# Kernel optimization log

Hardware: AMD Instinct MI355X
Metric: run time of the kernel (lower is better)

## Reference

```python
import jax, jax.numpy as jnp
import numpy as np
from jax.scipy.special import logsumexp

SCALE = 10.0
EPS = 1e-05
MARGIN_INTRA = 40.0
MARGIN_INTER = 6.0
K_INTRA = 4   # sorted1[4:]
K_INTER = 6   # sorted2[6:]


def setup_inputs() -> dict:
    key = jax.random.key(0)
    k1, k2 = jax.random.split(key)
    n, d, n_cams = 4096, 256, 8
    feature = jax.random.normal(k1, (n, d), dtype=jnp.float32)
    camid = jax.random.randint(k2, (n,), 0, n_cams, dtype=jnp.int64)
    return {"feature": feature, "camid": camid}


def reference(feature, camid):
    n = feature.shape[0]
    # pairwise Euclidean distances: ||fi||^2 + ||fj||^2 - 2 fi.fj + eps, clamped, sqrt
    sq = jnp.sum(feature * feature, axis=1)                      # [n]
    dist = sq[:, None] + sq[None, :] + EPS - 2.0 * (feature @ feature.T)
    dist = jnp.sqrt(jnp.clip(dist, 1e-12))                       # [n, n]

    same_cam = camid[:, None] == camid[None, :]                  # [n, n] bool
    inf = jnp.array(jnp.inf, dtype=dist.dtype)

    # masked sorts: +inf padding sorts to the end and contributes exp(-inf)=0
    sorted_intra = jnp.sort(jnp.where(same_cam, dist, inf), axis=1)   # [n, n]
    sorted_inter = jnp.sort(jnp.where(same_cam, inf, dist), axis=1)   # [n, n]

    # x = log(sum(exp(-scale * sorted[:1]))) == -scale * sorted[0]
    x_intra = -SCALE * sorted_intra[:, 0]
    y_intra = logsumexp(-SCALE * sorted_intra[:, K_INTRA:], axis=1)
    x_inter = -SCALE * sorted_inter[:, 0]
    y_inter = logsumexp(-SCALE * sorted_inter[:, K_INTER:], axis=1)

    loss_intra = jnp.sum(jnp.maximum(-x_intra + y_intra + MARGIN_INTRA, 0.0))
    loss_inter = jnp.sum(jnp.maximum(-x_inter + y_inter + MARGIN_INTER, 0.0))
    return (loss_intra + 0.5 * loss_inter) / n
```

## Files before the change

kernel.cpp:

```cpp
#include <hip/hip_runtime.h>
#include <hip/hip_bf16.h>
#include <math.h>

#define N 4096
#define D 256
#define SCALEF 10.0f
#define EPSF 1e-5f
#define MARGIN_INTRA 40.0f
#define MARGIN_INTER 6.0f
#define K_INTRA 4
#define K_INTER 6

typedef unsigned short ushort_t;
typedef __attribute__((ext_vector_type(8))) short short8;
typedef __attribute__((ext_vector_type(4))) float floatx4;

__device__ __forceinline__ ushort_t f2bf(float x) {
    __hip_bfloat16 h = __float2bfloat16(x);
    return *reinterpret_cast<ushort_t*>(&h);
}
__device__ __forceinline__ float bf2f(ushort_t u) {
    __hip_bfloat16 h = *reinterpret_cast<__hip_bfloat16*>(&u);
    return __bfloat162float(h);
}

__global__ __launch_bounds__(64) void sqnorm_kernel(const float* __restrict__ F,
                                                    float* __restrict__ sq) {
    int row = blockIdx.x;
    int lane = threadIdx.x;
    float4 v = ((const float4*)(F + (size_t)row * D))[lane];
    float s = v.x * v.x + v.y * v.y + v.z * v.z + v.w * v.w;
#pragma unroll
    for (int off = 32; off > 0; off >>= 1) s += __shfl_down(s, off, 64);
    if (lane == 0) sq[row] = s;
}

__global__ __launch_bounds__(256) void prep_bf16(const float* __restrict__ F,
                                                 ushort_t* __restrict__ Fhi,
                                                 ushort_t* __restrict__ Flo) {
    int g = blockIdx.x * 256 + threadIdx.x;
    float4 v = ((const float4*)F)[g];
    ushort4 h, l;
    h.x = f2bf(v.x); l.x = f2bf(v.x - bf2f(h.x));
    h.y = f2bf(v.y); l.y = f2bf(v.y - bf2f(h.y));
    h.z = f2bf(v.z); l.z = f2bf(v.z - bf2f(h.z));
    h.w = f2bf(v.w); l.w = f2bf(v.w - bf2f(h.w));
    ((ushort4*)Fhi)[g] = h;
    ((ushort4*)Flo)[g] = l;
}

#define LDST 40

__global__ __launch_bounds__(256) void dist_gemm_mfma(const ushort_t* __restrict__ Fhi,
                                                      const ushort_t* __restrict__ Flo,
                                                      const float* __restrict__ sq,
                                                      float* __restrict__ dist) {
    __shared__ ushort_t lds[4][128 * LDST];
    int tid = threadIdx.x;
    int i0 = blockIdx.y * 128, j0 = blockIdx.x * 128;
    int wave = tid >> 6, lane = tid & 63;
    int wr = wave >> 1, wc = wave & 1;
    int lane15 = lane & 15, quad = lane >> 4;

    floatx4 acc[4][4] = {};

    int srow = tid >> 1, shalf = tid & 1;
    const ushort_t* gAh = Fhi + (size_t)(i0 + srow) * D + shalf * 16;
    const ushort_t* gAl = Flo + (size_t)(i0 + srow) * D + shalf * 16;
    const ushort_t* gBh = Fhi + (size_t)(j0 + srow) * D + shalf * 16;
    const ushort_t* gBl = Flo + (size_t)(j0 + srow) * D + shalf * 16;
    ushort_t* sdst = &lds[0][0] + srow * LDST + shalf * 16;

#pragma unroll 1
    for (int kt = 0; kt < 8; ++kt) {
        int koff = kt * 32;
        short8 ra[2], rb[2], rc[2], rd[2];
#pragma unroll
        for (int q = 0; q < 2; ++q) {
            ra[q] = *(const short8*)(gAh + koff + q * 8);
            rb[q] = *(const short8*)(gAl + koff + q * 8);
            rc[q] = *(const short8*)(gBh + koff + q * 8);
            rd[q] = *(const short8*)(gBl + koff + q * 8);
        }
        __syncthreads();
#pragma unroll
        for (int q = 0; q < 2; ++q) {
            *(short8*)(sdst + 0 * 128 * LDST + q * 8) = ra[q];
            *(short8*)(sdst + 1 * 128 * LDST + q * 8) = rb[q];
            *(short8*)(sdst + 2 * 128 * LDST + q * 8) = rc[q];
            *(short8*)(sdst + 3 * 128 * LDST + q * 8) = rd[q];
        }
        __syncthreads();

        short8 ahi[4], alo[4], bhi[4], blo[4];
        int eoff = quad * 8;
#pragma unroll
        for (int mi = 0; mi < 4; ++mi) {
            int r = wr * 64 + mi * 16 + lane15;
            ahi[mi] = *(const short8*)(&lds[0][0] + r * LDST + eoff);
            alo[mi] = *(const short8*)(&lds[1][0] + r * LDST + eoff);
        }
#pragma unroll
        for (int ni = 0; ni < 4; ++ni) {
            int r = wc * 64 + ni * 16 + lane15;
            bhi[ni] = *(const short8*)(&lds[2][0] + r * LDST + eoff);
            blo[ni] = *(const short8*)(&lds[3][0] + r * LDST + eoff);
        }
#pragma unroll
        for (int mi = 0; mi < 4; ++mi)
#pragma unroll
            for (int ni = 0; ni < 4; ++ni) {
                acc[mi][ni] = __builtin_amdgcn_mfma_f32_16x16x32_bf16(ahi[mi], bhi[ni], acc[mi][ni], 0, 0, 0);
                acc[mi][ni] = __builtin_amdgcn_mfma_f32_16x16x32_bf16(ahi[mi], blo[ni], acc[mi][ni], 0, 0, 0);
                acc[mi][ni] = __builtin_amdgcn_mfma_f32_16x16x32_bf16(alo[mi], bhi[ni], acc[mi][ni], 0, 0, 0);
            }
    }

#pragma unroll
    for (int mi = 0; mi < 4; ++mi) {
        int ibase = i0 + wr * 64 + mi * 16 + quad * 4;
        float si[4];
#pragma unroll
        for (int r = 0; r < 4; ++r) si[r] = sq[ibase + r];
#pragma unroll
        for (int ni = 0; ni < 4; ++ni) {
            int j = j0 + wc * 64 + ni * 16 + lane15;
            float sj = sq[j];
#pragma unroll
            for (int r = 0; r < 4; ++r) {
                float d2 = si[r] + sj + EPSF - 2.0f * acc[mi][ni][r];
                dist[(size_t)(ibase + r) * N + j] = sqrtf(fmaxf(d2, 1e-12f));
            }
        }
    }
}

#define BM 64
#define BN 64
#define BK 16
__global__ __launch_bounds__(256) void dist_gemm(const float* __restrict__ F,
                                                 const float* __restrict__ sq,
                                                 float* __restrict__ dist) {
    __shared__ float As[BK][BM];
    __shared__ float Bs[BK][BN];
    int tid = threadIdx.x;
    int i0 = blockIdx.y * BM;
    int j0 = blockIdx.x * BN;
    int tx = tid & 15, ty = tid >> 4;
    float acc[4][4] = {};
    int lr = tid >> 2, kq = tid & 3;
    for (int kt = 0; kt < D; kt += BK) {
        float4 a = *(const float4*)(F + (size_t)(i0 + lr) * D + kt + kq * 4);
        float4 b = *(const float4*)(F + (size_t)(j0 + lr) * D + kt + kq * 4);
        __syncthreads();
        As[kq * 4 + 0][lr] = a.x; As[kq * 4 + 1][lr] = a.y;
        As[kq * 4 + 2][lr] = a.z; As[kq * 4 + 3][lr] = a.w;
        Bs[kq * 4 + 0][lr] = b.x; Bs[kq * 4 + 1][lr] = b.y;
        Bs[kq * 4 + 2][lr] = b.z; Bs[kq * 4 + 3][lr] = b.w;
        __syncthreads();
#pragma unroll
        for (int kk = 0; kk < BK; ++kk) {
            float av[4], bv[4];
            *(float4*)av = *(const float4*)&As[kk][ty * 4];
            *(float4*)bv = *(const float4*)&Bs[kk][tx * 4];
#pragma unroll
            for (int mi = 0; mi < 4; ++mi)
#pragma unroll
                for (int ni = 0; ni < 4; ++ni) acc[mi][ni] += av[mi] * bv[ni];
        }
    }
#pragma unroll
    for (int mi = 0; mi < 4; ++mi) {
        int i = i0 + ty * 4 + mi;
        float s_i = sq[i];
#pragma unroll
        for (int ni = 0; ni < 4; ++ni) {
            int j = j0 + tx * 4 + ni;
            float d2 = s_i + sq[j] + EPSF - 2.0f * acc[mi][ni];
            dist[(size_t)i * N + j] = sqrtf(fmaxf(d2, 1e-12f));
        }
    }
}

template <int L>
__device__ __forceinline__ void bubble_insert(float (&t)[L], float v) {
#pragma unroll
    for (int q = 0; q < L; ++q) {
        float hi = fmaxf(t[q], v);
        v = fminf(t[q], v);
        t[q] = hi;
    }
}

template <int L>
__device__ __forceinline__ void merge_sorted(float (&a)[L], const float (&b)[L]) {
    float c[L];
#pragma unroll
    for (int k = 0; k < L; ++k) {
        float m = fmaxf(a[k], b[k]);
#pragma unroll
        for (int i = 1; i <= k; ++i) m = fmaxf(m, fminf(a[i - 1], b[k - i]));
        c[k] = m;
    }
#pragma unroll
    for (int k = 0; k < L; ++k) a[k] = c[k];
}

__global__ __launch_bounds__(256) void rowloss2(const float* __restrict__ dist,
                                                const int* __restrict__ camid,
                                                float* __restrict__ rowloss) {
    int wave = threadIdx.x >> 6, lane = threadIdx.x & 63;
    int row = blockIdx.x * 4 + wave;
    const float4* dr4 = (const float4*)(dist + (size_t)row * N);
    const int4* cam4 = (const int4*)camid;
    const int ci = camid[row];

    float tI[K_INTRA + 1], tX[K_INTER + 1];
#pragma unroll
    for (int q = 0; q <= K_INTRA; ++q) tI[q] = -INFINITY;
#pragma unroll
    for (int q = 0; q <= K_INTER; ++q) tX[q] = -INFINITY;

#pragma unroll 1
    for (int s = 0; s < 16; ++s) {
        float4 d4 = dr4[s * 64 + lane];
        int4 c4 = cam4[s * 64 + lane];
        float lg;
        bool ii;
        lg = -SCALEF * d4.x; ii = (c4.x == ci);
        bubble_insert(tI, ii ? lg : -INFINITY); bubble_insert(tX, ii ? -INFINITY : lg);
        lg = -SCALEF * d4.y; ii = (c4.y == ci);
        bubble_insert(tI, ii ? lg : -INFINITY); bubble_insert(tX, ii ? -INFINITY : lg);
        lg = -SCALEF * d4.z; ii = (c4.z == ci);
        bubble_insert(tI, ii ? lg : -INFINITY); bubble_insert(tX, ii ? -INFINITY : lg);
        lg = -SCALEF * d4.w; ii = (c4.w == ci);
        bubble_insert(tI, ii ? lg : -INFINITY); bubble_insert(tX, ii ? -INFINITY : lg);
    }

#pragma unroll
    for (int off = 32; off >= 1; off >>= 1) {
        float oI[K_INTRA + 1], oX[K_INTER + 1];
#pragma unroll
        for (int q = 0; q <= K_INTRA; ++q) oI[q] = __shfl_xor(tI[q], off, 64);
        merge_sorted(tI, oI);
#pragma unroll
        for (int q = 0; q <= K_INTER; ++q) oX[q] = __shfl_xor(tX[q], off, 64);
        merge_sorted(tX, oX);
    }
    float x0I = tI[0], shI = tI[K_INTRA];
    float x0X = tX[0], shX = tX[K_INTER];

    float sI = 0.0f, sX = 0.0f;
    int eqI = 0, gtI = 0, eqX = 0, gtX = 0;
#pragma unroll 1
    for (int s = 0; s < 16; ++s) {
        float4 d4 = dr4[s * 64 + lane];
        int4 c4 = cam4[s * 64 + lane];
        float lgs[4] = {-SCALEF * d4.x, -SCALEF * d4.y, -SCALEF * d4.z, -SCALEF * d4.w};
        int cms[4] = {c4.x, c4.y, c4.z, c4.w};
#pragma unroll
        for (int c = 0; c < 4; ++c) {
            bool ii = (cms[c] == ci);
            float vI = ii ? lgs[c] : -INFINITY;
            float vX = ii ? -INFINITY : lgs[c];
            if (vI < shI) sI += __expf(vI - shI);
            eqI += (vI == shI); gtI += (vI > shI);
            if (vX < shX) sX += __expf(vX - shX);
            eqX += (vX == shX); gtX += (vX > shX);
        }
    }
#pragma unroll
    for (int off = 32; off >= 1; off >>= 1) {
        sI += __shfl_xor(sI, off, 64);
        sX += __shfl_xor(sX, off, 64);
        eqI += __shfl_xor(eqI, off, 64);
        gtI += __shfl_xor(gtI, off, 64);
        eqX += __shfl_xor(eqX, off, 64);
        gtX += __shfl_xor(gtX, off, 64);
    }
    if (lane == 0) {
        float h1 = 0.0f, h2 = 0.0f;
        if (shI > -INFINITY) {
            float rest = sI + (float)(eqI - (K_INTRA - gtI));
            h1 = fmaxf(shI + logf(rest) - x0I + MARGIN_INTRA, 0.0f);
        }
        if (shX > -INFINITY) {
            float rest = sX + (float)(eqX - (K_INTER - gtX));
            h2 = fmaxf(shX + logf(rest) - x0X + MARGIN_INTER, 0.0f);
        }
        rowloss[row] = h1 + 0.5f * h2;
    }
}

__global__ __launch_bounds__(256) void final_reduce(const float* __restrict__ rowloss,
                                                    float* __restrict__ out) {
    __shared__ float sbuf[256];
    int tid = threadIdx.x;
    float acc = 0.0f;
#pragma unroll
    for (int s = 0; s < 16; ++s) acc += rowloss[tid + s * 256];
    sbuf[tid] = acc;
    __syncthreads();
    for (int stride = 128; stride > 0; stride >>= 1) {
        if (tid < stride) sbuf[tid] += sbuf[tid + stride];
        __syncthreads();
    }
    if (tid == 0) out[0] = sbuf[0] * (1.0f / (float)N);
}

extern "C" void kernel_launch(void* const* d_in, const int* in_sizes, int n_in,
                              void* d_out, int out_size, void* d_ws, size_t ws_size,
                              hipStream_t stream) {
    const float* F = (const float*)d_in[0];
    const int* camid = (const int*)d_in[1];
    float* out = (float*)d_out;
    char* ws = (char*)d_ws;
    const size_t DIST_BYTES = (size_t)N * N * 4;
    float* dist = (float*)ws;
    float* sq = (float*)(ws + DIST_BYTES);
    float* rowloss = (float*)(ws + DIST_BYTES + 16384);
    ushort_t* Fhi = (ushort_t*)(ws + DIST_BYTES + 32768);
    ushort_t* Flo = Fhi + (size_t)N * D;
    const size_t needed = DIST_BYTES + 32768 + 2 * (size_t)N * D * sizeof(ushort_t);

    sqnorm_kernel<<<N, 64, 0, stream>>>(F, sq);
    if (ws_size >= needed) {
        prep_bf16<<<(N * D / 4) / 256, 256, 0, stream>>>(F, Fhi, Flo);
        dist_gemm_mfma<<<dim3(N / 128, N / 128), 256, 0, stream>>>(Fhi, Flo, sq, dist);
    } else {
        dist_gemm<<<dim3(N / BN, N / BM), 256, 0, stream>>>(F, sq, dist);
    }
    rowloss2<<<N / 4, 256, 0, stream>>>(dist, camid, rowloss);
    final_reduce<<<1, 256, 0, stream>>>(rowloss, out);
}
```

Before: 139.2 us.

## Fuse distance GEMM with per-row top-k and logsumexp partials, drop dist matrix

```diff
diff --git a/kernel.cpp b/kernel.cpp
--- a/kernel.cpp
+++ b/kernel.cpp
@@ -8,8 +8,11 @@
 #define EPSF 1e-5f
 #define MARGIN_INTRA 40.0f
 #define MARGIN_INTER 6.0f
-#define K_INTRA 4
-#define K_INTER 6
+#define LI 3
+#define LX 6
+#define NCHUNK 16
+#define NSTRIP 32
+#define PPARTS (NCHUNK * 2)
 
 typedef unsigned short ushort_t;
 typedef __attribute__((ext_vector_type(8))) short short8;
@@ -24,272 +27,224 @@
     return __bfloat162float(h);
 }
 
-__global__ __launch_bounds__(64) void sqnorm_kernel(const float* __restrict__ F,
-                                                    float* __restrict__ sq) {
+template <int L>
+__device__ __forceinline__ void bubble_insert(float (&t)[L], float v) {
+#pragma unroll
+    for (int q = 0; q < L; ++q) {
+        float hi = fmaxf(t[q], v);
+        v = fminf(t[q], v);
+        t[q] = hi;
+    }
+}
+
+__global__ __launch_bounds__(64) void prep_kernel(const float* __restrict__ F,
+                                                  ushort_t* __restrict__ Fhi,
+                                                  ushort_t* __restrict__ Flo,
+                                                  float* __restrict__ sq,
+                                                  float* __restrict__ Rrow) {
     int row = blockIdx.x;
     int lane = threadIdx.x;
     float4 v = ((const float4*)(F + (size_t)row * D))[lane];
-    float s = v.x * v.x + v.y * v.y + v.z * v.z + v.w * v.w;
-#pragma unroll
-    for (int off = 32; off > 0; off >>= 1) s += __shfl_down(s, off, 64);
-    if (lane == 0) sq[row] = s;
-}
-
-__global__ __launch_bounds__(256) void prep_bf16(const float* __restrict__ F,
-                                                 ushort_t* __restrict__ Fhi,
-                                                 ushort_t* __restrict__ Flo) {
-    int g = blockIdx.x * 256 + threadIdx.x;
-    float4 v = ((const float4*)F)[g];
     ushort4 h, l;
     h.x = f2bf(v.x); l.x = f2bf(v.x - bf2f(h.x));
     h.y = f2bf(v.y); l.y = f2bf(v.y - bf2f(h.y));
     h.z = f2bf(v.z); l.z = f2bf(v.z - bf2f(h.z));
     h.w = f2bf(v.w); l.w = f2bf(v.w - bf2f(h.w));
-    ((ushort4*)Fhi)[g] = h;
-    ((ushort4*)Flo)[g] = l;
+    ((ushort4*)(Fhi + (size_t)row * D))[lane] = h;
+    ((ushort4*)(Flo + (size_t)row * D))[lane] = l;
+    float s = v.x * v.x + v.y * v.y + v.z * v.z + v.w * v.w;
+#pragma unroll
+    for (int off = 32; off > 0; off >>= 1) s += __shfl_down(s, off, 64);
+    if (lane == 0) {
+        sq[row] = s;
+        Rrow[row] = -SCALEF * sqrtf(2.0f * s);
+    }
 }
 
 #define LDST 40
 
-__global__ __launch_bounds__(256) void dist_gemm_mfma(const ushort_t* __restrict__ Fhi,
-                                                      const ushort_t* __restrict__ Flo,
-                                                      const float* __restrict__ sq,
-                                                      float* __restrict__ dist) {
+__global__ __launch_bounds__(256, 2) void fused_kernel(
+    const ushort_t* __restrict__ Fhi, const ushort_t* __restrict__ Flo,
+    const float* __restrict__ sq, const float* __restrict__ Rrow,
+    const int* __restrict__ camid,
+    float4* __restrict__ partA, float4* __restrict__ partB, float4* __restrict__ partC) {
     __shared__ ushort_t lds[4][128 * LDST];
     int tid = threadIdx.x;
-    int i0 = blockIdx.y * 128, j0 = blockIdx.x * 128;
     int wave = tid >> 6, lane = tid & 63;
     int wr = wave >> 1, wc = wave & 1;
     int lane15 = lane & 15, quad = lane >> 4;
-
-    floatx4 acc[4][4] = {};
+    int cid = blockIdx.x, sid = blockIdx.y;
+    int i0 = sid * 128, j00 = cid * 256;
+
+    float si[4], Ri4[4];
+    int ci4[4], ig[4];
+#pragma unroll
+    for (int ni = 0; ni < 4; ++ni) {
+        int i = i0 + wc * 64 + ni * 16 + lane15;
+        ig[ni] = i;
+        si[ni] = sq[i];
+        Ri4[ni] = Rrow[i];
+        ci4[ni] = camid[i];
+    }
+
+    float tI[4][LI], tX[4][LX], sIa[4], sXa[4];
+#pragma unroll
+    for (int ni = 0; ni < 4; ++ni) {
+#pragma unroll
+        for (int q = 0; q < LI; ++q) tI[ni][q] = -INFINITY;
+#pragma unroll
+        for (int q = 0; q < LX; ++q) tX[ni][q] = -INFINITY;
+        sIa[ni] = 0.0f; sXa[ni] = 0.0f;
+    }
 
     int srow = tid >> 1, shalf = tid & 1;
-    const ushort_t* gAh = Fhi + (size_t)(i0 + srow) * D + shalf * 16;
-    const ushort_t* gAl = Flo + (size_t)(i0 + srow) * D + shalf * 16;
-    const ushort_t* gBh = Fhi + (size_t)(j0 + srow) * D + shalf * 16;
-    const ushort_t* gBl = Flo + (size_t)(j0 + srow) * D + shalf * 16;
+    const ushort_t* gBh = Fhi + (size_t)(i0 + srow) * D + shalf * 16;
+    const ushort_t* gBl = Flo + (size_t)(i0 + srow) * D + shalf * 16;
     ushort_t* sdst = &lds[0][0] + srow * LDST + shalf * 16;
 
 #pragma unroll 1
-    for (int kt = 0; kt < 8; ++kt) {
-        int koff = kt * 32;
-        short8 ra[2], rb[2], rc[2], rd[2];
-#pragma unroll
-        for (int q = 0; q < 2; ++q) {
-            ra[q] = *(const short8*)(gAh + koff + q * 8);
-            rb[q] = *(const short8*)(gAl + koff + q * 8);
-            rc[q] = *(const short8*)(gBh + koff + q * 8);
-            rd[q] = *(const short8*)(gBl + koff + q * 8);
-        }
-        __syncthreads();
-#pragma unroll
-        for (int q = 0; q < 2; ++q) {
-            *(short8*)(sdst + 0 * 128 * LDST + q * 8) = ra[q];
-            *(short8*)(sdst + 1 * 128 * LDST + q * 8) = rb[q];
-            *(short8*)(sdst + 2 * 128 * LDST + q * 8) = rc[q];
-            *(short8*)(sdst + 3 * 128 * LDST + q * 8) = rd[q];
-        }
-        __syncthreads();
-
-        short8 ahi[4], alo[4], bhi[4], blo[4];
-        int eoff = quad * 8;
+    for (int jt = 0; jt < 2; ++jt) {
+        int j0 = j00 + jt * 128;
+        const ushort_t* gAh = Fhi + (size_t)(j0 + srow) * D + shalf * 16;
+        const ushort_t* gAl = Flo + (size_t)(j0 + srow) * D + shalf * 16;
+        floatx4 acc[4][4] = {};
+
+#pragma unroll 1
+        for (int kt = 0; kt < 8; ++kt) {
+            int koff = kt * 32;
+            short8 ra[2], rb[2], rc[2], rd[2];
+#pragma unroll
+            for (int q = 0; q < 2; ++q) {
+                ra[q] = *(const short8*)(gAh + koff + q * 8);
+                rb[q] = *(const short8*)(gAl + koff + q * 8);
+                rc[q] = *(const short8*)(gBh + koff + q * 8);
+                rd[q] = *(const short8*)(gBl + koff + q * 8);
+            }
+            __syncthreads();
+#pragma unroll
+            for (int q = 0; q < 2; ++q) {
+                *(short8*)(sdst + 0 * 128 * LDST + q * 8) = ra[q];
+                *(short8*)(sdst + 1 * 128 * LDST + q * 8) = rb[q];
+                *(short8*)(sdst + 2 * 128 * LDST + q * 8) = rc[q];
+                *(short8*)(sdst + 3 * 128 * LDST + q * 8) = rd[q];
+            }
+            __syncthreads();
+
+            short8 ahi[4], alo[4], bhi[4], blo[4];
+            int eoff = quad * 8;
+#pragma unroll
+            for (int mi = 0; mi < 4; ++mi) {
+                int r = wr * 64 + mi * 16 + lane15;
+                ahi[mi] = *(const short8*)(&lds[0][0] + r * LDST + eoff);
+                alo[mi] = *(const short8*)(&lds[1][0] + r * LDST + eoff);
+            }
+#pragma unroll
+            for (int ni = 0; ni < 4; ++ni) {
+                int r = wc * 64 + ni * 16 + lane15;
+                bhi[ni] = *(const short8*)(&lds[2][0] + r * LDST + eoff);
+                blo[ni] = *(const short8*)(&lds[3][0] + r * LDST + eoff);
+            }
+#pragma unroll
+            for (int mi = 0; mi < 4; ++mi)
+#pragma unroll
+                for (int ni = 0; ni < 4; ++ni) {
+                    acc[mi][ni] = __builtin_amdgcn_mfma_f32_16x16x32_bf16(ahi[mi], bhi[ni], acc[mi][ni], 0, 0, 0);
+                    acc[mi][ni] = __builtin_amdgcn_mfma_f32_16x16x32_bf16(ahi[mi], blo[ni], acc[mi][ni], 0, 0, 0);
+                    acc[mi][ni] = __builtin_amdgcn_mfma_f32_16x16x32_bf16(alo[mi], bhi[ni], acc[mi][ni], 0, 0, 0);
+                }
+        }
+
 #pragma unroll
         for (int mi = 0; mi < 4; ++mi) {
-            int r = wr * 64 + mi * 16 + lane15;
-            ahi[mi] = *(const short8*)(&lds[0][0] + r * LDST + eoff);
-            alo[mi] = *(const short8*)(&lds[1][0] + r * LDST + eoff);
-        }
+            int jg0 = j0 + wr * 64 + mi * 16 + quad * 4;
+            float4 sj4 = *(const float4*)(sq + jg0);
+            int4 cj4 = *(const int4*)(camid + jg0);
+            const float* sjp = (const float*)&sj4;
+            const int* cjp = (const int*)&cj4;
+#pragma unroll
+            for (int ni = 0; ni < 4; ++ni) {
+                int dd = jg0 - ig[ni];
+#pragma unroll
+                for (int r = 0; r < 4; ++r) {
+                    float d2 = si[ni] + sjp[r] + EPSF - 2.0f * acc[mi][ni][r];
+                    float d = sqrtf(fmaxf(d2, 1e-12f));
+                    float x = -SCALEF * d;
+                    float e = __expf(x - Ri4[ni]);
+                    bool ii = (cjp[r] == ci4[ni]);
+                    bool dg = ((dd + r) == 0);
+                    bool okI = ii && !dg;
+                    sIa[ni] += okI ? e : 0.0f;
+                    sXa[ni] += ii ? 0.0f : e;
+                    bubble_insert<LI>(tI[ni], okI ? x : -INFINITY);
+                    bubble_insert<LX>(tX[ni], ii ? -INFINITY : x);
+                }
+            }
+        }
+    }
+
+#pragma unroll
+    for (int off = 16; off <= 32; off <<= 1) {
 #pragma unroll
         for (int ni = 0; ni < 4; ++ni) {
-            int r = wc * 64 + ni * 16 + lane15;
-            bhi[ni] = *(const short8*)(&lds[2][0] + r * LDST + eoff);
-            blo[ni] = *(const short8*)(&lds[3][0] + r * LDST + eoff);
-        }
-#pragma unroll
-        for (int mi = 0; mi < 4; ++mi)
-#pragma unroll
-            for (int ni = 0; ni < 4; ++ni) {
-                acc[mi][ni] = __builtin_amdgcn_mfma_f32_16x16x32_bf16(ahi[mi], bhi[ni], acc[mi][ni], 0, 0, 0);
-                acc[mi][ni] = __builtin_amdgcn_mfma_f32_16x16x32_bf16(ahi[mi], blo[ni], acc[mi][ni], 0, 0, 0);
-                acc[mi][ni] = __builtin_amdgcn_mfma_f32_16x16x32_bf16(alo[mi], bhi[ni], acc[mi][ni], 0, 0, 0);
-            }
-    }
-
-#pragma unroll
-    for (int mi = 0; mi < 4; ++mi) {
-        int ibase = i0 + wr * 64 + mi * 16 + quad * 4;
-        float si[4];
-#pragma unroll
-        for (int r = 0; r < 4; ++r) si[r] = sq[ibase + r];
+            sIa[ni] += __shfl_xor(sIa[ni], off, 64);
+            sXa[ni] += __shfl_xor(sXa[ni], off, 64);
+            float oI[LI], oX[LX];
+#pragma unroll
+            for (int q = 0; q < LI; ++q) oI[q] = __shfl_xor(tI[ni][q], off, 64);
+#pragma unroll
+            for (int q = 0; q < LX; ++q) oX[q] = __shfl_xor(tX[ni][q], off, 64);
+#pragma unroll
+            for (int q = 0; q < LI; ++q) bubble_insert<LI>(tI[ni], oI[q]);
+#pragma unroll
+            for (int q = 0; q < LX; ++q) bubble_insert<LX>(tX[ni], oX[q]);
+        }
+    }
+
+    if (quad == 0) {
+        int p = cid * 2 + wr;
 #pragma unroll
         for (int ni = 0; ni < 4; ++ni) {
-            int j = j0 + wc * 64 + ni * 16 + lane15;
-            float sj = sq[j];
-#pragma unroll
-            for (int r = 0; r < 4; ++r) {
-                float d2 = si[r] + sj + EPSF - 2.0f * acc[mi][ni][r];
-                dist[(size_t)(ibase + r) * N + j] = sqrtf(fmaxf(d2, 1e-12f));
-            }
-        }
-    }
-}
-
-#define BM 64
-#define BN 64
-#define BK 16
-__global__ __launch_bounds__(256) void dist_gemm(const float* __restrict__ F,
-                                                 const float* __restrict__ sq,
-                                                 float* __restrict__ dist) {
-    __shared__ float As[BK][BM];
-    __shared__ float Bs[BK][BN];
-    int tid = threadIdx.x;
-    int i0 = blockIdx.y * BM;
-    int j0 = blockIdx.x * BN;
-    int tx = tid & 15, ty = tid >> 4;
-    float acc[4][4] = {};
-    int lr = tid >> 2, kq = tid & 3;
-    for (int kt = 0; kt < D; kt += BK) {
-        float4 a = *(const float4*)(F + (size_t)(i0 + lr) * D + kt + kq * 4);
-        float4 b = *(const float4*)(F + (size_t)(j0 + lr) * D + kt + kq * 4);
-        __syncthreads();
-        As[kq * 4 + 0][lr] = a.x; As[kq * 4 + 1][lr] = a.y;
-        As[kq * 4 + 2][lr] = a.z; As[kq * 4 + 3][lr] = a.w;
-        Bs[kq * 4 + 0][lr] = b.x; Bs[kq * 4 + 1][lr] = b.y;
-        Bs[kq * 4 + 2][lr] = b.z; Bs[kq * 4 + 3][lr] = b.w;
-        __syncthreads();
-#pragma unroll
-        for (int kk = 0; kk < BK; ++kk) {
-            float av[4], bv[4];
-            *(float4*)av = *(const float4*)&As[kk][ty * 4];
-            *(float4*)bv = *(const float4*)&Bs[kk][tx * 4];
-#pragma unroll
-            for (int mi = 0; mi < 4; ++mi)
-#pragma unroll
-                for (int ni = 0; ni < 4; ++ni) acc[mi][ni] += av[mi] * bv[ni];
-        }
-    }
-#pragma unroll
-    for (int mi = 0; mi < 4; ++mi) {
-        int i = i0 + ty * 4 + mi;
-        float s_i = sq[i];
-#pragma unroll
-        for (int ni = 0; ni < 4; ++ni) {
-            int j = j0 + tx * 4 + ni;
-            float d2 = s_i + sq[j] + EPSF - 2.0f * acc[mi][ni];
-            dist[(size_t)i * N + j] = sqrtf(fmaxf(d2, 1e-12f));
-        }
-    }
-}
-
-template <int L>
-__device__ __forceinline__ void bubble_insert(float (&t)[L], float v) {
-#pragma unroll
-    for (int q = 0; q < L; ++q) {
-        float hi = fmaxf(t[q], v);
-        v = fminf(t[q], v);
-        t[q] = hi;
-    }
-}
-
-template <int L>
-__device__ __forceinline__ void merge_sorted(float (&a)[L], const float (&b)[L]) {
-    float c[L];
-#pragma unroll
-    for (int k = 0; k < L; ++k) {
-        float m = fmaxf(a[k], b[k]);
-#pragma unroll
-        for (int i = 1; i <= k; ++i) m = fmaxf(m, fminf(a[i - 1], b[k - i]));
-        c[k] = m;
-    }
-#pragma unroll
-    for (int k = 0; k < L; ++k) a[k] = c[k];
-}
-
-__global__ __launch_bounds__(256) void rowloss2(const float* __restrict__ dist,
-                                                const int* __restrict__ camid,
-                                                float* __restrict__ rowloss) {
-    int wave = threadIdx.x >> 6, lane = threadIdx.x & 63;
-    int row = blockIdx.x * 4 + wave;
-    const float4* dr4 = (const float4*)(dist + (size_t)row * N);
-    const int4* cam4 = (const int4*)camid;
-    const int ci = camid[row];
-
-    float tI[K_INTRA + 1], tX[K_INTER + 1];
-#pragma unroll
-    for (int q = 0; q <= K_INTRA; ++q) tI[q] = -INFINITY;
-#pragma unroll
-    for (int q = 0; q <= K_INTER; ++q) tX[q] = -INFINITY;
-
+            size_t idx = (size_t)p * N + ig[ni];
+            partA[idx] = make_float4(tI[ni][0], tI[ni][1], tI[ni][2], sIa[ni]);
+            partB[idx] = make_float4(tX[ni][0], tX[ni][1], tX[ni][2], tX[ni][3]);
+            partC[idx] = make_float4(tX[ni][4], tX[ni][5], sXa[ni], 0.0f);
+        }
+    }
+}
+
+__global__ __launch_bounds__(256) void merge_kernel(const float4* __restrict__ partA,
+                                                    const float4* __restrict__ partB,
+                                                    const float4* __restrict__ partC,
+                                                    const float* __restrict__ Rrow,
+                                                    float* __restrict__ rowloss) {
+    int row = blockIdx.x * 256 + threadIdx.x;
+    float mI[LI] = {-INFINITY, -INFINITY, -INFINITY};
+    float mX[LX] = {-INFINITY, -INFINITY, -INFINITY, -INFINITY, -INFINITY, -INFINITY};
+    float SI = 0.0f, SX = 0.0f;
 #pragma unroll 1
-    for (int s = 0; s < 16; ++s) {
-        float4 d4 = dr4[s * 64 + lane];
-        int4 c4 = cam4[s * 64 + lane];
-        float lg;
-        bool ii;
-        lg = -SCALEF * d4.x; ii = (c4.x == ci);
-        bubble_insert(tI, ii ? lg : -INFINITY); bubble_insert(tX, ii ? -INFINITY : lg);
-        lg = -SCALEF * d4.y; ii = (c4.y == ci);
-        bubble_insert(tI, ii ? lg : -INFINITY); bubble_insert(tX, ii ? -INFINITY : lg);
-        lg = -SCALEF * d4.z; ii = (c4.z == ci);
-        bubble_insert(tI, ii ? lg : -INFINITY); bubble_insert(tX, ii ? -INFINITY : lg);
-        lg = -SCALEF * d4.w; ii = (c4.w == ci);
-        bubble_insert(tI, ii ? lg : -INFINITY); bubble_insert(tX, ii ? -INFINITY : lg);
-    }
-
-#pragma unroll
-    for (int off = 32; off >= 1; off >>= 1) {
-        float oI[K_INTRA + 1], oX[K_INTER + 1];
-#pragma unroll
-        for (int q = 0; q <= K_INTRA; ++q) oI[q] = __shfl_xor(tI[q], off, 64);
-        merge_sorted(tI, oI);
-#pragma unroll
-        for (int q = 0; q <= K_INTER; ++q) oX[q] = __shfl_xor(tX[q], off, 64);
-        merge_sorted(tX, oX);
-    }
-    float x0I = tI[0], shI = tI[K_INTRA];
-    float x0X = tX[0], shX = tX[K_INTER];
-
-    float sI = 0.0f, sX = 0.0f;
-    int eqI = 0, gtI = 0, eqX = 0, gtX = 0;
-#pragma unroll 1
-    for (int s = 0; s < 16; ++s) {
-        float4 d4 = dr4[s * 64 + lane];
-        int4 c4 = cam4[s * 64 + lane];
-        float lgs[4] = {-SCALEF * d4.x, -SCALEF * d4.y, -SCALEF * d4.z, -SCALEF * d4.w};
-        int cms[4] = {c4.x, c4.y, c4.z, c4.w};
-#pragma unroll
-        for (int c = 0; c < 4; ++c) {
-            bool ii = (cms[c] == ci);
-            float vI = ii ? lgs[c] : -INFINITY;
-            float vX = ii ? -INFINITY : lgs[c];
-            if (vI < shI) sI += __expf(vI - shI);
-            eqI += (vI == shI); gtI += (vI > shI);
-            if (vX < shX) sX += __expf(vX - shX);
-            eqX += (vX == shX); gtX += (vX > shX);
-        }
-    }
-#pragma unroll
-    for (int off = 32; off >= 1; off >>= 1) {
-        sI += __shfl_xor(sI, off, 64);
-        sX += __shfl_xor(sX, off, 64);
-        eqI += __shfl_xor(eqI, off, 64);
-        gtI += __shfl_xor(gtI, off, 64);
-        eqX += __shfl_xor(eqX, off, 64);
-        gtX += __shfl_xor(gtX, off, 64);
-    }
-    if (lane == 0) {
-        float h1 = 0.0f, h2 = 0.0f;
-        if (shI > -INFINITY) {
-            float rest = sI + (float)(eqI - (K_INTRA - gtI));
-            h1 = fmaxf(shI + logf(rest) - x0I + MARGIN_INTRA, 0.0f);
-        }
-        if (shX > -INFINITY) {
-            float rest = sX + (float)(eqX - (K_INTER - gtX));
-            h2 = fmaxf(shX + logf(rest) - x0X + MARGIN_INTER, 0.0f);
-        }
-        rowloss[row] = h1 + 0.5f * h2;
-    }
+    for (int p = 0; p < PPARTS; ++p) {
+        size_t idx = (size_t)p * N + row;
+        float4 a = partA[idx];
+        float4 b = partB[idx];
+        float4 c = partC[idx];
+        bubble_insert<LI>(mI, a.x); bubble_insert<LI>(mI, a.y); bubble_insert<LI>(mI, a.z);
+        SI += a.w;
+        bubble_insert<LX>(mX, b.x); bubble_insert<LX>(mX, b.y);
+        bubble_insert<LX>(mX, b.z); bubble_insert<LX>(mX, b.w);
+        bubble_insert<LX>(mX, c.x); bubble_insert<LX>(mX, c.y);
+        SX += c.z;
+    }
+    float R = Rrow[row];
+    float subI = __expf(mI[0] - R) + __expf(mI[1] - R) + __expf(mI[2] - R);
+    float restI = fmaxf(SI - subI, 1e-37f);
+    float yI = R + logf(restI);
+    float hI = fmaxf(yI + SCALEF * sqrtf(EPSF) + MARGIN_INTRA, 0.0f);
+    float subX = __expf(mX[0] - R) + __expf(mX[1] - R) + __expf(mX[2] - R) +
+                 __expf(mX[3] - R) + __expf(mX[4] - R) + __expf(mX[5] - R);
+    float restX = fmaxf(SX - subX, 1e-37f);
+    float yX = R + logf(restX);
+    float hX = fmaxf(-mX[0] + yX + MARGIN_INTER, 0.0f);
+    rowloss[row] = hI + 0.5f * hX;
 }
 
 __global__ __launch_bounds__(256) void final_reduce(const float* __restrict__ rowloss,
@@ -315,21 +270,19 @@
     const int* camid = (const int*)d_in[1];
     float* out = (float*)d_out;
     char* ws = (char*)d_ws;
-    const size_t DIST_BYTES = (size_t)N * N * 4;
-    float* dist = (float*)ws;
-    float* sq = (float*)(ws + DIST_BYTES);
-    float* rowloss = (float*)(ws + DIST_BYTES + 16384);
-    ushort_t* Fhi = (ushort_t*)(ws + DIST_BYTES + 32768);
+
+    ushort_t* Fhi = (ushort_t*)ws;
     ushort_t* Flo = Fhi + (size_t)N * D;
-    const size_t needed = DIST_BYTES + 32768 + 2 * (size_t)N * D * sizeof(ushort_t);
-
-    sqnorm_kernel<<<N, 64, 0, stream>>>(F, sq);
-    if (ws_size >= needed) {
-        prep_bf16<<<(N * D / 4) / 256, 256, 0, stream>>>(F, Fhi, Flo);
-        dist_gemm_mfma<<<dim3(N / 128, N / 128), 256, 0, stream>>>(Fhi, Flo, sq, dist);
-    } else {
-        dist_gemm<<<dim3(N / BN, N / BM), 256, 0, stream>>>(F, sq, dist);
-    }
-    rowloss2<<<N / 4, 256, 0, stream>>>(dist, camid, rowloss);
+    float* sq = (float*)(ws + 2 * (size_t)N * D * 2);
+    float* Rrow = sq + N;
+    float* rowloss = Rrow + N;
+    float4* partA = (float4*)(ws + 2 * (size_t)N * D * 2 + 3 * N * 4);
+    float4* partB = partA + (size_t)PPARTS * N;
+    float4* partC = partB + (size_t)PPARTS * N;
+
+    prep_kernel<<<N, 64, 0, stream>>>(F, Fhi, Flo, sq, Rrow);
+    fused_kernel<<<dim3(NCHUNK, NSTRIP), 256, 0, stream>>>(Fhi, Flo, sq, Rrow, camid,
+                                                           partA, partB, partC);
+    merge_kernel<<<N / 256, 256, 0, stream>>>(partA, partB, partC, Rrow, rowloss);
     final_reduce<<<1, 256, 0, stream>>>(rowloss, out);
 }
```

Measured after the change: 130.3 us. 1.07x faster.
